# Kernel optimization log

Hardware: AMD Instinct MI355X
Metric: run time of the kernel (lower is better)

The kernel has to match this reference:

```python
import jax, jax.numpy as jnp
import numpy as np

STRIDE = 1
PADDING = 1
GROUPS = 1


def setup_inputs() -> dict:
    key = jax.random.key(0)
    kx, kw, kb = jax.random.split(key, 3)
    x_int = jax.random.randint(kx, (16, 256, 56, 56), 0, 127, dtype=jnp.int32)
    weight_int = jax.random.randint(kw, (256, 256, 3, 3), 0, 127, dtype=jnp.int32)
    bias_int = jax.random.randint(kb, (256,), 0, 127, dtype=jnp.int32)
    return {"x_int": x_int, "weight_int": weight_int, "bias_int": bias_int}


def reference(x_int, weight_int, bias_int):
    # Integer conv2d with int32 accumulation, exactly F.conv2d semantics.
    y = jax.lax.conv_general_dilated(
        x_int,
        weight_int,
        window_strides=(STRIDE, STRIDE),
        padding=((PADDING, PADDING), (PADDING, PADDING)),
        dimension_numbers=("NCHW", "OIHW", "NCHW"),
        feature_group_count=GROUPS,
    )
    # bias broadcast over [B, Cout, H, W]
    return y + bias_int[None, :, None, None]
```

## Files before the change

### kernel.cpp

```cpp
#include <hip/hip_runtime.h>


typedef int v4i  __attribute__((ext_vector_type(4)));
typedef int v16i __attribute__((ext_vector_type(16)));

#define X8_ROWSTRIDE 1856
#define X8_IMGSTRIDE 107648
#define X8_BYTES     13778944
#define W8_CHUNK     18432
#define XS_OFF       55296
#define XS_BUF       30720

typedef const __attribute__((address_space(1))) unsigned char* gptr_t;
typedef __attribute__((address_space(3))) unsigned char* lptr_t;

__device__ __forceinline__ int pack4(const int* p, int stride) {
  return (p[0] & 255) | ((p[stride] & 255) << 8) |
         ((p[2 * stride] & 255) << 16) | ((p[3 * stride] & 255) << 24);
}

__global__ __launch_bounds__(256)
void pack_all(const int* __restrict__ x, const int* __restrict__ wgt,
              unsigned char* __restrict__ ws8) {
  const int blk = blockIdx.x;
  if (blk < 784) {
    const int gid = blk * 256 + threadIdx.x;
    const int srcg = gid & 1;
    int t = gid >> 1;
    const int sq = t % 14;  t /= 14;
    const int row = t % 56 + 1;
    const int cb  = t / 56;
    const int chunk = cb >> 4, b = cb & 15;
    const int ci0 = chunk * 32 + srcg * 16;
    const int* src = x + (b * 256 + ci0) * 3136 + (row - 1) * 56 + 4 * sq;
    v4i L[16];
    #pragma unroll
    for (int ch = 0; ch < 16; ++ch) L[ch] = *(const v4i*)(src + ch * 3136);
    unsigned char* dstrow = ws8 + cb * X8_IMGSTRIDE + row * X8_ROWSTRIDE;
    #pragma unroll
    for (int j = 0; j < 4; ++j) {
      const int slot = 4 * sq + 1 + j;
      v4i g;
      #pragma unroll
      for (int d = 0; d < 4; ++d)
        g[d] = (L[4 * d][j] & 255) | ((L[4 * d + 1][j] & 255) << 8) |
               ((L[4 * d + 2][j] & 255) << 16) | ((L[4 * d + 3][j] & 255) << 24);
      const int p = (srcg + (slot >> 2)) & 1;
      *(v4i*)(dstrow + slot * 32 + p * 16) = g;
    }
  } else if (blk < 1012) {
    const int g2 = (blk - 784) * 256 + threadIdx.x;
    const int cb = g2 / 456;
    const int r  = g2 - cb * 456;
    int off;
    if (r < 232) {
      const int row = r < 116 ? 0 : 57;
      const int rr = r % 116;
      off = row * X8_ROWSTRIDE + (rr >> 1) * 32 + (rr & 1) * 16;
    } else {
      const int r2 = r - 232;
      const int row = (r2 >> 2) + 1;
      const int slot = (r2 & 2) ? 57 : 0;
      off = row * X8_ROWSTRIDE + slot * 32 + (r2 & 1) * 16;
    }
    *(v4i*)(ws8 + cb * X8_IMGSTRIDE + off) = (v4i){0, 0, 0, 0};
  } else {
    const int gw = (blk - 1012) * 256 + threadIdx.x;
    const int p = gw & 1;
    int t = gw >> 1;
    const int tap = t % 9;  t /= 9;
    const int co = t & 63;
    const int tcc = t >> 6;
    const int chunk = tcc & 7, cotile = tcc >> 3;
    const int srcg = (p + (co >> 2)) & 1;
    const int ci0 = chunk * 32 + srcg * 16;
    const int* src = wgt + ((cotile * 64 + co) * 256 + ci0) * 9 + tap;
    v4i v = (v4i){pack4(src, 9), pack4(src + 36, 9),
                  pack4(src + 72, 9), pack4(src + 108, 9)};
    *(v4i*)(ws8 + X8_BYTES + (t * 9 + tap) * 32 + p * 16) = v;
  }
}

__device__ __forceinline__ void stage_chunk(const unsigned char* wg,
                                            const unsigned char* xg,
                                            unsigned char* ldsb, int c, int buf,
                                            int tid) {
  const unsigned char* wsrc = wg + c * W8_CHUNK;
  const unsigned char* xsrc = xg + c * (16 * X8_IMGSTRIDE);
  unsigned char* wdst = ldsb + buf * W8_CHUNK;
  unsigned char* xdst = ldsb + XS_OFF + buf * XS_BUF;
  #pragma unroll
  for (int i = 0; i < 2; ++i) {
    const int o = (tid + i * 512) * 16;
    __builtin_amdgcn_global_load_lds((gptr_t)(wsrc + o), (lptr_t)(wdst + o), 16, 0, 0);
  }
  if (tid < 128) {
    const int o = (1024 + tid) * 16;
    __builtin_amdgcn_global_load_lds((gptr_t)(wsrc + o), (lptr_t)(wdst + o), 16, 0, 0);
  } else {
    const int o = (tid - 128) * 16;
    __builtin_amdgcn_global_load_lds((gptr_t)(xsrc + o), (lptr_t)(xdst + o), 16, 0, 0);
  }
  #pragma unroll
  for (int i = 0; i < 3; ++i) {
    const int o = (384 + tid + i * 512) * 16;
    __builtin_amdgcn_global_load_lds((gptr_t)(xsrc + o), (lptr_t)(xdst + o), 16, 0, 0);
  }
}

__global__ __launch_bounds__(512, 2)
void conv_main(const unsigned char* __restrict__ ws8, const int* __restrict__ bias,
               int* __restrict__ out) {
  __shared__ __align__(16) unsigned char lds[3 * W8_CHUNK + 3 * XS_BUF];
  __shared__ int bls[64];

  const int tid = threadIdx.x, lane = tid & 63, wv = tid >> 6;
  const int n = lane & 31, gq = lane >> 5;
  const int tc = blockIdx.y;
  const int hb = blockIdx.x;
  const int hg = hb >> 4, b = hb & 15;
  const int h0 = hg * 14;

  if (tid < 64) {
    bls[tid] = bias[tc * 64 + tid];
    asm volatile("s_waitcnt lgkmcnt(0)" ::: "memory");
  }

  const int abase = n * 288 + (((gq + (n >> 2)) & 1) << 4);
  int boff[3][4];
  #pragma unroll
  for (int kw = 0; kw < 3; ++kw)
    #pragma unroll
    for (int bt = 0; bt < 4; ++bt) {
      int slot = bt * 16 + (n & 15) + kw;
      if (slot > 57) slot = 57;
      boff[kw][bt] = slot * 32 + (((gq + (slot >> 2)) & 1) << 4);
    }
  const int rbase = (2 * wv + (n >> 4)) * X8_ROWSTRIDE;

  v16i acc[2][4];
  #pragma unroll
  for (int i = 0; i < 2; ++i)
    #pragma unroll
    for (int j = 0; j < 4; ++j)
      acc[i][j] = (v16i){0,0,0,0,0,0,0,0,0,0,0,0,0,0,0,0};

  const unsigned char* wg = ws8 + X8_BYTES + tc * (8 * W8_CHUNK);
  const unsigned char* xg = ws8 + b * X8_IMGSTRIDE + h0 * X8_ROWSTRIDE;

  stage_chunk(wg, xg, lds, 0, 0, tid);
  stage_chunk(wg, xg, lds, 1, 1, tid);
  int buf = 0, nbuf = 2;
  for (int c = 0; c < 8; ++c) {
    if (c < 7) asm volatile("s_waitcnt vmcnt(6)" ::: "memory");
    else       asm volatile("s_waitcnt vmcnt(0)" ::: "memory");
    __builtin_amdgcn_s_barrier();
    asm volatile("" ::: "memory");
    if (c < 6) stage_chunk(wg, xg, lds, c + 2, nbuf, tid);
    if (wv < 7) {
      const unsigned char* wls = lds + buf * W8_CHUNK;
      const unsigned char* xs  = lds + XS_OFF + buf * XS_BUF;
      #pragma unroll
      for (int kh = 0; kh < 3; ++kh) {
        const unsigned char* xr = xs + rbase + kh * X8_ROWSTRIDE;
        #pragma unroll
        for (int kw = 0; kw < 3; ++kw) {
          const int tap = kh * 3 + kw;
          const v4i a0 = *(const v4i*)(wls + abase + tap * 32);
          const v4i a1 = *(const v4i*)(wls + 9216 + abase + tap * 32);
          #pragma unroll
          for (int bt = 0; bt < 4; ++bt) {
            const v4i bb = *(const v4i*)(xr + boff[kw][bt]);
            acc[0][bt] = __builtin_amdgcn_mfma_i32_32x32x32_i8(a0, bb, acc[0][bt], 0, 0, 0);
            acc[1][bt] = __builtin_amdgcn_mfma_i32_32x32x32_i8(a1, bb, acc[1][bt], 0, 0, 0);
          }
        }
      }
    }
    buf  = (buf  == 2) ? 0 : buf  + 1;
    nbuf = (nbuf == 2) ? 0 : nbuf + 1;
  }

  if (wv >= 7) return;
  const int h = h0 + 2 * wv + (n >> 4);
  const int wbase = lane & 15;
  #pragma unroll
  for (int ct = 0; ct < 2; ++ct) {
    #pragma unroll
    for (int r = 0; r < 16; ++r) {
      const int co64 = ct * 32 + (r & 3) + 8 * (r >> 2) + 4 * gq;
      const int bv = bls[co64];
      int* orow = out + ((b * 256 + tc * 64 + co64) * 56 + h) * 56;
      #pragma unroll
      for (int bt = 0; bt < 4; ++bt) {
        const int w0 = bt * 16 + wbase;
        if (w0 < 56) orow[w0] = acc[ct][bt][r] + bv;
      }
    }
  }
}

extern "C" void kernel_launch(void* const* d_in, const int* in_sizes, int n_in,
                              void* d_out, int out_size, void* d_ws, size_t ws_size,
                              hipStream_t stream) {
  const int* x    = (const int*)d_in[0];
  const int* w    = (const int*)d_in[1];
  const int* bias = (const int*)d_in[2];
  unsigned char* ws8 = (unsigned char*)d_ws;
  hipLaunchKernelGGL(pack_all, dim3(1156), dim3(256), 0, stream, x, w, ws8);
  hipLaunchKernelGGL(conv_main, dim3(64, 4, 1), dim3(512), 0, stream,
                     ws8, bias, (int*)d_out);
}
```

Baseline: 132.1 us.

## Retile conv to 128 output channels by 8 rows per block with double buffering

Each block of the main conv kernel now covers 128 output channels and 8 output rows with 4 waves, where it used to cover 64 channels and 14 rows with 8 waves (7 doing work). Every wave now holds a 4x4 grid of MFMA accumulators, so each loaded input fragment is reused across four weight fragments. The LDS pipeline drops from triple to double buffering, with an extra barrier after compute. The grid grows to 224 blocks at one block per CU, which raises per-wave register pressure and lowers occupancy and latency hiding.

```diff
diff --git a/kernel.cpp b/kernel.cpp
--- a/kernel.cpp
+++ b/kernel.cpp
@@ -8,11 +8,17 @@
 #define X8_IMGSTRIDE 107648
 #define X8_BYTES     13778944
 #define W8_CHUNK     18432
-#define XS_OFF       55296
-#define XS_BUF       30720
+#define W8_COTILE    147456
+#define WBUF         36864
+#define XBUF         20480
+#define LBUF         57344
 
 typedef const __attribute__((address_space(1))) unsigned char* gptr_t;
 typedef __attribute__((address_space(3))) unsigned char* lptr_t;
+
+__device__ __forceinline__ void gll(const unsigned char* g, unsigned char* l) {
+  __builtin_amdgcn_global_load_lds((gptr_t)g, (lptr_t)l, 16, 0, 0);
+}
 
 __device__ __forceinline__ int pack4(const int* p, int stride) {
   return (p[0] & 255) | ((p[stride] & 255) << 8) |
@@ -81,50 +87,55 @@
   }
 }
 
-__device__ __forceinline__ void stage_chunk(const unsigned char* wg,
+__device__ __forceinline__ void stage_chunk(const unsigned char* wa,
+                                            const unsigned char* wb,
                                             const unsigned char* xg,
                                             unsigned char* ldsb, int c, int buf,
                                             int tid) {
-  const unsigned char* wsrc = wg + c * W8_CHUNK;
+  const unsigned char* wsa = wa + c * W8_CHUNK;
+  const unsigned char* wsb = wb + c * W8_CHUNK;
   const unsigned char* xsrc = xg + c * (16 * X8_IMGSTRIDE);
-  unsigned char* wdst = ldsb + buf * W8_CHUNK;
-  unsigned char* xdst = ldsb + XS_OFF + buf * XS_BUF;
-  #pragma unroll
-  for (int i = 0; i < 2; ++i) {
-    const int o = (tid + i * 512) * 16;
-    __builtin_amdgcn_global_load_lds((gptr_t)(wsrc + o), (lptr_t)(wdst + o), 16, 0, 0);
+  unsigned char* wdst = ldsb + buf * LBUF;
+  unsigned char* xdst = wdst + WBUF;
+  #pragma unroll
+  for (int i = 0; i < 4; ++i) {
+    const int o = (tid + i * 256) * 16;
+    gll(wsa + o, wdst + o);
   }
   if (tid < 128) {
     const int o = (1024 + tid) * 16;
-    __builtin_amdgcn_global_load_lds((gptr_t)(wsrc + o), (lptr_t)(wdst + o), 16, 0, 0);
+    gll(wsa + o, wdst + o);
   } else {
     const int o = (tid - 128) * 16;
-    __builtin_amdgcn_global_load_lds((gptr_t)(xsrc + o), (lptr_t)(xdst + o), 16, 0, 0);
-  }
-  #pragma unroll
-  for (int i = 0; i < 3; ++i) {
-    const int o = (384 + tid + i * 512) * 16;
-    __builtin_amdgcn_global_load_lds((gptr_t)(xsrc + o), (lptr_t)(xdst + o), 16, 0, 0);
-  }
-}
-
-__global__ __launch_bounds__(512, 2)
+    gll(wsb + o, wdst + W8_CHUNK + o);
+  }
+  #pragma unroll
+  for (int i = 0; i < 4; ++i) {
+    const int o = (128 + tid + i * 256) * 16;
+    gll(wsb + o, wdst + W8_CHUNK + o);
+  }
+  #pragma unroll
+  for (int i = 0; i < 5; ++i) {
+    const int o = (tid + i * 256) * 16;
+    gll(xsrc + o, xdst + o);
+  }
+}
+
+__global__ __launch_bounds__(256, 1)
 void conv_main(const unsigned char* __restrict__ ws8, const int* __restrict__ bias,
                int* __restrict__ out) {
-  __shared__ __align__(16) unsigned char lds[3 * W8_CHUNK + 3 * XS_BUF];
-  __shared__ int bls[64];
+  __shared__ __align__(16) unsigned char lds[2 * LBUF];
+  __shared__ int bls[128];
 
   const int tid = threadIdx.x, lane = tid & 63, wv = tid >> 6;
   const int n = lane & 31, gq = lane >> 5;
   const int tc = blockIdx.y;
   const int hb = blockIdx.x;
   const int hg = hb >> 4, b = hb & 15;
-  const int h0 = hg * 14;
-
-  if (tid < 64) {
-    bls[tid] = bias[tc * 64 + tid];
-    asm volatile("s_waitcnt lgkmcnt(0)" ::: "memory");
-  }
+  const int h0 = hg * 8;
+
+  if (tid < 128) bls[tid] = bias[tc * 128 + tid];
+  asm volatile("s_waitcnt lgkmcnt(0)" ::: "memory");
 
   const int abase = n * 288 + (((gq + (n >> 2)) & 1) << 4);
   int boff[3][4];
@@ -138,63 +149,68 @@
     }
   const int rbase = (2 * wv + (n >> 4)) * X8_ROWSTRIDE;
 
-  v16i acc[2][4];
-  #pragma unroll
-  for (int i = 0; i < 2; ++i)
+  v16i acc[4][4];
+  #pragma unroll
+  for (int i = 0; i < 4; ++i)
     #pragma unroll
     for (int j = 0; j < 4; ++j)
       acc[i][j] = (v16i){0,0,0,0,0,0,0,0,0,0,0,0,0,0,0,0};
 
-  const unsigned char* wg = ws8 + X8_BYTES + tc * (8 * W8_CHUNK);
+  const unsigned char* wa = ws8 + X8_BYTES + (2 * tc) * W8_COTILE;
+  const unsigned char* wb = wa + W8_COTILE;
   const unsigned char* xg = ws8 + b * X8_IMGSTRIDE + h0 * X8_ROWSTRIDE;
 
-  stage_chunk(wg, xg, lds, 0, 0, tid);
-  stage_chunk(wg, xg, lds, 1, 1, tid);
-  int buf = 0, nbuf = 2;
+  stage_chunk(wa, wb, xg, lds, 0, 0, tid);
+  int buf = 0;
+  #pragma unroll 1
   for (int c = 0; c < 8; ++c) {
-    if (c < 7) asm volatile("s_waitcnt vmcnt(6)" ::: "memory");
-    else       asm volatile("s_waitcnt vmcnt(0)" ::: "memory");
+    if (c < 7) {
+      stage_chunk(wa, wb, xg, lds, c + 1, buf ^ 1, tid);
+      asm volatile("s_waitcnt vmcnt(14)" ::: "memory");
+    } else {
+      asm volatile("s_waitcnt vmcnt(0)" ::: "memory");
+    }
     __builtin_amdgcn_s_barrier();
     asm volatile("" ::: "memory");
-    if (c < 6) stage_chunk(wg, xg, lds, c + 2, nbuf, tid);
-    if (wv < 7) {
-      const unsigned char* wls = lds + buf * W8_CHUNK;
-      const unsigned char* xs  = lds + XS_OFF + buf * XS_BUF;
+    const unsigned char* wls = lds + buf * LBUF;
+    const unsigned char* xs  = wls + WBUF;
+    #pragma unroll
+    for (int kh = 0; kh < 3; ++kh) {
+      const unsigned char* xr = xs + rbase + kh * X8_ROWSTRIDE;
       #pragma unroll
-      for (int kh = 0; kh < 3; ++kh) {
-        const unsigned char* xr = xs + rbase + kh * X8_ROWSTRIDE;
+      for (int kw = 0; kw < 3; ++kw) {
+        const int tap = kh * 3 + kw;
+        v4i a[4];
         #pragma unroll
-        for (int kw = 0; kw < 3; ++kw) {
-          const int tap = kh * 3 + kw;
-          const v4i a0 = *(const v4i*)(wls + abase + tap * 32);
-          const v4i a1 = *(const v4i*)(wls + 9216 + abase + tap * 32);
+        for (int q = 0; q < 4; ++q)
+          a[q] = *(const v4i*)(wls + q * 9216 + abase + tap * 32);
+        #pragma unroll
+        for (int bt = 0; bt < 4; ++bt) {
+          const v4i bb = *(const v4i*)(xr + boff[kw][bt]);
           #pragma unroll
-          for (int bt = 0; bt < 4; ++bt) {
-            const v4i bb = *(const v4i*)(xr + boff[kw][bt]);
-            acc[0][bt] = __builtin_amdgcn_mfma_i32_32x32x32_i8(a0, bb, acc[0][bt], 0, 0, 0);
-            acc[1][bt] = __builtin_amdgcn_mfma_i32_32x32x32_i8(a1, bb, acc[1][bt], 0, 0, 0);
-          }
+          for (int q = 0; q < 4; ++q)
+            acc[q][bt] = __builtin_amdgcn_mfma_i32_32x32x32_i8(a[q], bb, acc[q][bt], 0, 0, 0);
         }
       }
     }
-    buf  = (buf  == 2) ? 0 : buf  + 1;
-    nbuf = (nbuf == 2) ? 0 : nbuf + 1;
-  }
-
-  if (wv >= 7) return;
+    asm volatile("" ::: "memory");
+    __builtin_amdgcn_s_barrier();
+    buf ^= 1;
+  }
+
   const int h = h0 + 2 * wv + (n >> 4);
   const int wbase = lane & 15;
   #pragma unroll
-  for (int ct = 0; ct < 2; ++ct) {
+  for (int q = 0; q < 4; ++q) {
     #pragma unroll
     for (int r = 0; r < 16; ++r) {
-      const int co64 = ct * 32 + (r & 3) + 8 * (r >> 2) + 4 * gq;
-      const int bv = bls[co64];
-      int* orow = out + ((b * 256 + tc * 64 + co64) * 56 + h) * 56;
+      const int co = q * 32 + (r & 3) + 8 * (r >> 2) + 4 * gq;
+      const int bv = bls[co];
+      int* orow = out + ((b * 256 + tc * 128 + co) * 56 + h) * 56;
       #pragma unroll
       for (int bt = 0; bt < 4; ++bt) {
         const int w0 = bt * 16 + wbase;
-        if (w0 < 56) orow[w0] = acc[ct][bt][r] + bv;
+        if (w0 < 56) orow[w0] = acc[q][bt][r] + bv;
       }
     }
   }
@@ -208,6 +224,6 @@
   const int* bias = (const int*)d_in[2];
   unsigned char* ws8 = (unsigned char*)d_ws;
   hipLaunchKernelGGL(pack_all, dim3(1156), dim3(256), 0, stream, x, w, ws8);
-  hipLaunchKernelGGL(conv_main, dim3(64, 4, 1), dim3(512), 0, stream,
+  hipLaunchKernelGGL(conv_main, dim3(112, 2, 1), dim3(256), 0, stream,
                      ws8, bias, (int*)d_out);
 }
```

Measured after the change: 152.4 us. +15.3%, slower.
